# Kernel optimization log

Hardware: AMD Instinct MI355X
Metric: run time of the kernel (lower is better)

The kernel has to match this reference:

```python
import jax, jax.numpy as jnp
import numpy as np

D_MODEL = 1024
D_STATE = 16
N_LAYERS = 2
EXPAND = 2
D_CONV = 4
D_INNER = EXPAND * D_MODEL
DT_RANK = D_MODEL // 16  # 64
B, L = 2, 1024


def setup_inputs() -> dict:
    key = jax.random.key(0)
    ks = jax.random.split(key, 8)
    rn = lambda k, shape, s: jax.random.normal(k, shape, jnp.float32) * s
    x = rn(ks[0], (B, L, D_MODEL), 1.0)
    in_proj_w = rn(ks[1], (N_LAYERS, 2 * D_INNER, D_MODEL), D_MODEL ** -0.5)
    conv_w = rn(ks[2], (N_LAYERS, D_INNER, 1, D_CONV), D_CONV ** -0.5)
    conv_b = jnp.zeros((N_LAYERS, D_INNER), jnp.float32)
    x_proj_w = rn(ks[3], (N_LAYERS, DT_RANK + 2 * D_STATE, D_INNER), D_INNER ** -0.5)
    dt_proj_w = rn(ks[4], (N_LAYERS, D_INNER, DT_RANK), DT_RANK ** -0.5)
    dt_proj_b = rn(ks[5], (N_LAYERS, D_INNER), 0.1)
    # canonical Mamba init: A = -exp(A_log), A_log = log(1..d_state)
    A_log = jnp.tile(jnp.log(jnp.arange(1, D_STATE + 1, dtype=jnp.float32)), (N_LAYERS, D_INNER, 1))
    Dp = jnp.ones((N_LAYERS, D_INNER), jnp.float32)
    out_proj_w = rn(ks[6], (N_LAYERS, D_MODEL, D_INNER), D_INNER ** -0.5)
    ln_g = jnp.ones((N_LAYERS, D_MODEL), jnp.float32)
    ln_b = jnp.zeros((N_LAYERS, D_MODEL), jnp.float32)
    fn_g = jnp.ones((D_MODEL,), jnp.float32)
    fn_b = jnp.zeros((D_MODEL,), jnp.float32)
    return dict(x=x, ln_g=ln_g, ln_b=ln_b, in_proj_w=in_proj_w, conv_w=conv_w,
                conv_b=conv_b, x_proj_w=x_proj_w, dt_proj_w=dt_proj_w,
                dt_proj_b=dt_proj_b, A_log=A_log, Dp=Dp, out_proj_w=out_proj_w,
                fn_g=fn_g, fn_b=fn_b)


def _ln(x, g, b):
    m = jnp.mean(x, -1, keepdims=True)
    v = jnp.mean((x - m) ** 2, -1, keepdims=True)
    return (x - m) * jax.lax.rsqrt(v + 1e-5) * g + b


def _mamba_block(x, in_w, cw, cb, xpw, dtw, dtb, A_log, Dp, ow):
    Bb = x.shape[0]
    # input projection -> [B, L, 2*d_inner]
    xz = jnp.einsum('bld,ed->ble', x, in_w)
    u, res = jnp.split(xz, 2, axis=-1)
    # causal depthwise conv over time (torch: padding=3 then [..., :L])
    uc = jax.lax.conv_general_dilated(
        u.transpose(0, 2, 1), cw, (1,), [(D_CONV - 1, 0)],
        dimension_numbers=('NCH', 'OIH', 'NCH'), feature_group_count=D_INNER)
    u = jax.nn.silu(uc.transpose(0, 2, 1) + cb)  # [B, L, d_inner]
    # input-dependent dt, B, C
    xdbl = jnp.einsum('ble,fe->blf', u, xpw)
    dt, Bc, Cc = jnp.split(xdbl, [DT_RANK, DT_RANK + D_STATE], axis=-1)
    delta = jax.nn.softplus(jnp.einsum('blr,dr->bld', dt, dtw) + dtb)  # [B,L,d_inner]
    A = -jnp.exp(A_log)  # [d_inner, d_state]

    def step(h, inp):
        d_t, B_t, C_t, u_t = inp  # [B,d_inner],[B,d_state],[B,d_state],[B,d_inner]
        h = jnp.exp(d_t[:, :, None] * A) * h + (d_t * u_t)[:, :, None] * B_t[:, None, :]
        y = jnp.einsum('bds,bs->bd', h, C_t)
        return h, y

    xs = (delta.transpose(1, 0, 2), Bc.transpose(1, 0, 2),
          Cc.transpose(1, 0, 2), u.transpose(1, 0, 2))
    h0 = jnp.zeros((Bb, D_INNER, D_STATE), x.dtype)
    _, ys = jax.lax.scan(step, h0, xs)
    y = ys.transpose(1, 0, 2) + u * Dp
    y = y * jax.nn.silu(res)
    return jnp.einsum('ble,de->bld', y, ow)


def reference(x, ln_g, ln_b, in_proj_w, conv_w, conv_b, x_proj_w, dt_proj_w,
              dt_proj_b, A_log, Dp, out_proj_w, fn_g, fn_b):
    for i in range(N_LAYERS):
        x = x + _mamba_block(_ln(x, ln_g[i], ln_b[i]), in_proj_w[i], conv_w[i],
                             conv_b[i], x_proj_w[i], dt_proj_w[i], dt_proj_b[i],
                             A_log[i], Dp[i], out_proj_w[i])
    # dropout is identity in eval mode
    return _ln(x, fn_g, fn_b)
```

## Files before the change

kernel.cpp:

```cpp
#include <hip/hip_runtime.h>
#include <hip/hip_bf16.h>
#include <math.h>
#include <stdint.h>

#define DMODEL 1024
#define DSTATE 16
#define DINNER 2048
#define DTRANK 64
#define NB 2
#define LSEQ 1024
#define ROWS (NB*LSEQ)
#define NCH 64
#define LCH (LSEQ/NCH)

typedef __bf16 bf16_t;
typedef __bf16 bf16x8 __attribute__((ext_vector_type(8)));
typedef __bf16 bf16x4 __attribute__((ext_vector_type(4)));
typedef float  f32x4  __attribute__((ext_vector_type(4)));

#define AS1(p) ((const __attribute__((address_space(1))) void*)(p))
#define AS3(p) ((__attribute__((address_space(3))) void*)(uint32_t)(uintptr_t)(p))

static __device__ __forceinline__ float sigmoidf_(float x){ return 1.f/(1.f+__expf(-x)); }
static __device__ __forceinline__ float softplusf_(float x){ return fmaxf(x,0.f) + log1pf(__expf(-fabsf(x))); }

__global__ __launch_bounds__(256) void cvt_kernel(const float* __restrict__ in,
    bf16_t* __restrict__ out, int n4)
{
  int i = blockIdx.x*256 + threadIdx.x;
  if (i < n4){
    float4 v = ((const float4*)in)[i];
    bf16x4 o = { (bf16_t)v.x, (bf16_t)v.y, (bf16_t)v.z, (bf16_t)v.w };
    ((bf16x4*)out)[i] = o;
  }
}

template<int OUTBF>
__global__ __launch_bounds__(256) void ln_kernel(const float* __restrict__ x,
    const float* __restrict__ g, const float* __restrict__ b,
    float* __restrict__ outf, bf16_t* __restrict__ outb)
{
  int row = blockIdx.x;
  float4 v = ((const float4*)(x + (size_t)row*DMODEL))[threadIdx.x];
  float s  = v.x+v.y+v.z+v.w;
  float s2 = v.x*v.x+v.y*v.y+v.z*v.z+v.w*v.w;
  #pragma unroll
  for (int off=32; off>=1; off>>=1){ s += __shfl_xor(s,off); s2 += __shfl_xor(s2,off); }
  __shared__ float red[8];
  int lane = threadIdx.x & 63, wid = threadIdx.x >> 6;
  if (lane==0){ red[wid]=s; red[4+wid]=s2; }
  __syncthreads();
  float ts  = red[0]+red[1]+red[2]+red[3];
  float ts2 = red[4]+red[5]+red[6]+red[7];
  float mean = ts*(1.f/DMODEL);
  float var  = ts2*(1.f/DMODEL) - mean*mean;
  float rstd = rsqrtf(var + 1e-5f);
  float4 gv = ((const float4*)g)[threadIdx.x];
  float4 bv = ((const float4*)b)[threadIdx.x];
  float4 o;
  o.x=(v.x-mean)*rstd*gv.x+bv.x;
  o.y=(v.y-mean)*rstd*gv.y+bv.y;
  o.z=(v.z-mean)*rstd*gv.z+bv.z;
  o.w=(v.w-mean)*rstd*gv.w+bv.w;
  if (OUTBF){
    bf16x4 ob = { (bf16_t)o.x, (bf16_t)o.y, (bf16_t)o.z, (bf16_t)o.w };
    ((bf16x4*)(outb + (size_t)row*DMODEL))[threadIdx.x] = ob;
  } else {
    ((float4*)(outf + (size_t)row*DMODEL))[threadIdx.x] = o;
  }
}

#define GBM 128
#define GBN 128
#define GBK 64

template<int EPI, bool NGUARD>
__global__ __launch_bounds__(256) void gemm_bf16(
    const bf16_t* __restrict__ A, int lda,
    const bf16_t* __restrict__ W, int ldw,
    float* __restrict__ C, int ldc,
    int M, int N, int K,
    const float* __restrict__ bias,
    const float* __restrict__ addsrc,
    bf16_t* __restrict__ C2)
{
  __shared__ __align__(16) char lds[2*GBM*GBK*2];
  char* sA = lds;
  char* sB = lds + GBM*GBK*2;
  const int tid  = threadIdx.x;
  const int lane = tid & 63, wid = tid >> 6;
  const int wr = wid >> 1, wc = wid & 1;
  const int frow = lane & 15, kgrp = lane >> 4;
  const int m0 = blockIdx.y*GBM, n0 = blockIdx.x*GBN;
  const int srow  = (lane >> 3);
  const int scolb = (lane & 7) * 16;

  f32x4 acc[4][4];
  #pragma unroll
  for (int i=0;i<4;i++)
    #pragma unroll
    for (int j=0;j<4;j++)
      acc[i][j] = (f32x4){0.f,0.f,0.f,0.f};

  for (int k0 = 0; k0 < K; k0 += GBK) {
    #pragma unroll
    for (int r=0;r<4;++r){
      int ci  = r*4 + wid;
      int row = ci*8 + srow;
      {
        const char* src = (const char*)A + ((size_t)(m0+row)*lda + k0)*2 + scolb;
        __builtin_amdgcn_global_load_lds(AS1(src), AS3(sA + ci*1024), 16, 0, 0);
      }
      {
        int grow = n0 + row;
        if (NGUARD) grow = (grow < N) ? grow : (N-1);
        const char* src = (const char*)W + ((size_t)grow*ldw + k0)*2 + scolb;
        __builtin_amdgcn_global_load_lds(AS1(src), AS3(sB + ci*1024), 16, 0, 0);
      }
    }
    __syncthreads();
    #pragma unroll
    for (int ks=0; ks<2; ++ks){
      bf16x8 af[4], bfr[4];
      #pragma unroll
      for (int i=0;i<4;i++)
        af[i] = *(const bf16x8*)(sA + (wr*64 + i*16 + frow)*128 + ks*64 + kgrp*16);
      #pragma unroll
      for (int j=0;j<4;j++)
        bfr[j] = *(const bf16x8*)(sB + (wc*64 + j*16 + frow)*128 + ks*64 + kgrp*16);
      #pragma unroll
      for (int i=0;i<4;i++)
        #pragma unroll
        for (int j=0;j<4;j++)
          acc[i][j] = __builtin_amdgcn_mfma_f32_16x16x32_bf16(af[i], bfr[j], acc[i][j], 0, 0, 0);
    }
    __syncthreads();
  }

  #pragma unroll
  for (int i=0;i<4;i++){
    int rbase = m0 + wr*64 + i*16 + kgrp*4;
    #pragma unroll
    for (int j=0;j<4;j++){
      int col = n0 + wc*64 + j*16 + frow;
      if (NGUARD && col >= N) continue;
      #pragma unroll
      for (int q=0;q<4;q++){
        float v = acc[i][j][q];
        int row = rbase + q;
        if (EPI==1) v = softplusf_(v + bias[col]);
        if (EPI==2) v += addsrc[(size_t)row*ldc + col];
        C[(size_t)row*ldc + col] = v;
        if (EPI==3) C2[(size_t)row*ldc + col] = (bf16_t)v;
      }
    }
  }
}

__global__ __launch_bounds__(256) void conv_silu_kernel(
    const float* __restrict__ xz, const float* __restrict__ cw,
    const float* __restrict__ cb, float* __restrict__ u, bf16_t* __restrict__ ub)
{
  int idx = blockIdx.x*256 + threadIdx.x;
  int d  = idx & (DINNER-1);
  int bl = idx >> 11;
  int l  = bl & (LSEQ-1);
  const float* col = xz + (size_t)bl*(2*DINNER) + d;
  float w0=cw[d*4+0], w1=cw[d*4+1], w2=cw[d*4+2], w3=cw[d*4+3];
  float x3 = col[0];
  float x2 = (l>=1) ? col[-(ptrdiff_t)(2*DINNER)]  : 0.f;
  float x1 = (l>=2) ? col[-(ptrdiff_t)(4*DINNER)]  : 0.f;
  float x0 = (l>=3) ? col[-(ptrdiff_t)(6*DINNER)]  : 0.f;
  float acc = cb[d] + w0*x0 + w1*x1 + w2*x2 + w3*x3;
  float uu = acc * sigmoidf_(acc);
  u [(size_t)bl*DINNER + d] = uu;
  ub[(size_t)bl*DINNER + d] = (bf16_t)uu;
}

__global__ __launch_bounds__(256) void scan_phase1(
    const float* __restrict__ delta, const float* __restrict__ u,
    const float* __restrict__ xdbl, const float* __restrict__ A_log,
    float* __restrict__ hout, float* __restrict__ sumd)
{
  int gid = blockIdx.x*256 + threadIdx.x;
  int d = gid & (DINNER-1);
  int c = (gid >> 11) & (NCH-1);
  int b = gid >> 17;
  float A[DSTATE];
  #pragma unroll
  for (int s=0;s<DSTATE;s++) A[s] = -__expf(A_log[d*DSTATE+s]);
  int l0 = c*LCH;
  const float* drow = delta + ((size_t)(b*LSEQ + l0))*DINNER + d;
  const float* urow = u     + ((size_t)(b*LSEQ + l0))*DINNER + d;
  const float* xrow = xdbl  + ((size_t)(b*LSEQ + l0))*96 + DTRANK;
  float h[DSTATE] = {};
  float sd = 0.f;
  for (int l=0; l<LCH; ++l) {
    float dv = drow[(size_t)l*DINNER];
    float uv = urow[(size_t)l*DINNER];
    const float* bc = xrow + l*96;
    float du = dv*uv;
    sd += dv;
    #pragma unroll
    for (int s=0;s<DSTATE;s++)
      h[s] = __expf(dv*A[s])*h[s] + du*bc[s];
  }
  float* hp = hout + (((size_t)(b*NCH + c))*DINNER + d)*DSTATE;
  #pragma unroll
  for (int q=0;q<4;q++)
    ((float4*)hp)[q] = make_float4(h[4*q],h[4*q+1],h[4*q+2],h[4*q+3]);
  sumd[((size_t)(b*NCH + c))*DINNER + d] = sd;
}

__global__ __launch_bounds__(256) void scan_phase2(
    float* __restrict__ hout, const float* __restrict__ sumd,
    const float* __restrict__ A_log)
{
  int gid = blockIdx.x*256 + threadIdx.x;
  int s = gid & (DSTATE-1);
  int d = (gid >> 4) & (DINNER-1);
  int b = gid >> 15;
  float A = -__expf(A_log[d*DSTATE+s]);
  float h = 0.f;
  for (int c=0; c<NCH; ++c) {
    size_t hi = (((size_t)(b*NCH + c))*DINNER + d)*DSTATE + s;
    float tmp = hout[hi];
    hout[hi] = h;
    float P = __expf(A * sumd[((size_t)(b*NCH + c))*DINNER + d]);
    h = P*h + tmp;
  }
}

__global__ __launch_bounds__(256) void scan_phase3(
    const float* __restrict__ delta, bf16_t* __restrict__ ysb,
    const float* __restrict__ u,
    const float* __restrict__ xz,
    const float* __restrict__ xdbl,
    const float* __restrict__ A_log,
    const float* __restrict__ Dp,
    const float* __restrict__ hin)
{
  int gid = blockIdx.x*256 + threadIdx.x;
  int d = gid & (DINNER-1);
  int c = (gid >> 11) & (NCH-1);
  int b = gid >> 17;
  float A[DSTATE];
  #pragma unroll
  for (int s=0;s<DSTATE;s++) A[s] = -__expf(A_log[d*DSTATE+s]);
  float Dpd = Dp[d];
  float h[DSTATE];
  const float* hp = hin + (((size_t)(b*NCH + c))*DINNER + d)*DSTATE;
  #pragma unroll
  for (int q=0;q<4;q++){
    float4 hv = ((const float4*)hp)[q];
    h[4*q]=hv.x; h[4*q+1]=hv.y; h[4*q+2]=hv.z; h[4*q+3]=hv.w;
  }
  int l0 = c*LCH;
  const float* drow = delta + ((size_t)(b*LSEQ + l0))*DINNER + d;
  const float* urow = u     + ((size_t)(b*LSEQ + l0))*DINNER + d;
  const float* rrow = xz    + ((size_t)(b*LSEQ + l0))*2*DINNER + DINNER + d;
  const float* xrow = xdbl  + ((size_t)(b*LSEQ + l0))*96 + DTRANK;
  bf16_t* yrow = ysb + ((size_t)(b*LSEQ + l0))*DINNER + d;
  for (int l=0; l<LCH; ++l) {
    float dv = drow[(size_t)l*DINNER];
    float uv = urow[(size_t)l*DINNER];
    float rv = rrow[(size_t)l*2*DINNER];
    const float* bc = xrow + l*96;
    float du = dv*uv;
    float y = 0.f;
    #pragma unroll
    for (int s=0;s<DSTATE;s++){
      float dA = __expf(dv*A[s]);
      h[s] = dA*h[s] + du*bc[s];
      y += h[s]*bc[DSTATE+s];
    }
    y = (y + uv*Dpd) * (rv * sigmoidf_(rv));
    yrow[(size_t)l*DINNER] = (bf16_t)y;
  }
}

extern "C" void kernel_launch(void* const* d_in, const int* in_sizes, int n_in,
                              void* d_out, int out_size, void* d_ws, size_t ws_size,
                              hipStream_t stream)
{
  const float* x      = (const float*)d_in[0];
  const float* ln_g   = (const float*)d_in[1];
  const float* ln_b   = (const float*)d_in[2];
  const float* in_w   = (const float*)d_in[3];
  const float* conv_w = (const float*)d_in[4];
  const float* conv_b = (const float*)d_in[5];
  const float* xp_w   = (const float*)d_in[6];
  const float* dt_w   = (const float*)d_in[7];
  const float* dt_b   = (const float*)d_in[8];
  const float* A_log  = (const float*)d_in[9];
  const float* Dp     = (const float*)d_in[10];
  const float* out_w  = (const float*)d_in[11];
  const float* fn_g   = (const float*)d_in[12];
  const float* fn_b   = (const float*)d_in[13];
  float* out = (float*)d_out;

  char* p = (char*)d_ws;
  auto alloc = [&](size_t bytes)->char*{ char* r = p; p += (bytes + 255) & ~(size_t)255; return r; };

  const size_t N_INW = (size_t)2*2*DINNER*DMODEL;
  const size_t N_XPW = (size_t)2*96*DINNER;
  const size_t N_DTW = (size_t)2*DINNER*DTRANK;
  const size_t N_OUTW= (size_t)2*DMODEL*DINNER;

  bf16_t* inw_b  = (bf16_t*)alloc(N_INW*2);
  bf16_t* xpw_b  = (bf16_t*)alloc(N_XPW*2);
  bf16_t* dtw_b  = (bf16_t*)alloc(N_DTW*2);
  bf16_t* outw_b = (bf16_t*)alloc(N_OUTW*2);
  float*  x_cur  = (float*) alloc((size_t)ROWS*DMODEL*4);
  bf16_t* xn_b   = (bf16_t*)alloc((size_t)ROWS*DMODEL*2);
  float*  xz     = (float*) alloc((size_t)ROWS*2*DINNER*4);
  float*  ubuf   = (float*) alloc((size_t)ROWS*DINNER*4);
  bf16_t* ub_b   = (bf16_t*)alloc((size_t)ROWS*DINNER*2);
  float*  xdbl   = (float*) alloc((size_t)ROWS*96*4);
  bf16_t* xdbl_b = (bf16_t*)alloc((size_t)ROWS*96*2);
  float*  delta  = (float*) alloc((size_t)ROWS*DINNER*4);
  float*  hout   = (float*) alloc((size_t)NB*NCH*DINNER*DSTATE*4);
  float*  sumd   = (float*) alloc((size_t)NB*NCH*DINNER*4);
  bf16_t* ys_b   = ub_b;

  cvt_kernel<<<(int)((N_INW/4 +255)/256),256,0,stream>>>(in_w,  inw_b,  (int)(N_INW/4));
  cvt_kernel<<<(int)((N_XPW/4 +255)/256),256,0,stream>>>(xp_w,  xpw_b,  (int)(N_XPW/4));
  cvt_kernel<<<(int)((N_DTW/4 +255)/256),256,0,stream>>>(dt_w,  dtw_b,  (int)(N_DTW/4));
  cvt_kernel<<<(int)((N_OUTW/4+255)/256),256,0,stream>>>(out_w, outw_b, (int)(N_OUTW/4));

  for (int layer=0; layer<2; ++layer) {
    const float* xin = (layer==0) ? x : x_cur;
    const float* Al  = A_log + (size_t)layer*DINNER*DSTATE;
    ln_kernel<1><<<ROWS,256,0,stream>>>(xin, ln_g+layer*DMODEL, ln_b+layer*DMODEL, nullptr, xn_b);
    gemm_bf16<0,false><<<dim3(2*DINNER/GBN, ROWS/GBM),256,0,stream>>>(
        xn_b, DMODEL, inw_b + (size_t)layer*2*DINNER*DMODEL, DMODEL,
        xz, 2*DINNER, ROWS, 2*DINNER, DMODEL, nullptr, nullptr, nullptr);
    conv_silu_kernel<<<(ROWS*DINNER)/256,256,0,stream>>>(
        xz, conv_w + (size_t)layer*DINNER*4, conv_b + (size_t)layer*DINNER, ubuf, ub_b);
    gemm_bf16<3,true><<<dim3(1, ROWS/GBM),256,0,stream>>>(
        ub_b, DINNER, xpw_b + (size_t)layer*96*DINNER, DINNER,
        xdbl, 96, ROWS, 96, DINNER, nullptr, nullptr, xdbl_b);
    gemm_bf16<1,false><<<dim3(DINNER/GBN, ROWS/GBM),256,0,stream>>>(
        xdbl_b, 96, dtw_b + (size_t)layer*DINNER*DTRANK, DTRANK,
        delta, DINNER, ROWS, DINNER, DTRANK,
        dt_b + (size_t)layer*DINNER, nullptr, nullptr);
    scan_phase1<<<(NB*NCH*DINNER)/256,256,0,stream>>>(delta, ubuf, xdbl, Al, hout, sumd);
    scan_phase2<<<(NB*DINNER*DSTATE)/256,256,0,stream>>>(hout, sumd, Al);
    scan_phase3<<<(NB*NCH*DINNER)/256,256,0,stream>>>(
        delta, ys_b, ubuf, xz, xdbl, Al, Dp + (size_t)layer*DINNER, hout);
    gemm_bf16<2,false><<<dim3(DMODEL/GBN, ROWS/GBM),256,0,stream>>>(
        ys_b, DINNER, outw_b + (size_t)layer*DMODEL*DINNER, DINNER,
        x_cur, DMODEL, ROWS, DMODEL, DINNER, nullptr, xin, nullptr);
  }
  ln_kernel<0><<<ROWS,256,0,stream>>>(x_cur, fn_g, fn_b, out, nullptr);
}
```

Measured before the change: 541.2 us.

## Store xz and u in bf16, split-K x_proj, swizzle GEMM blocks, halve scan chunks

```diff
diff --git a/kernel.cpp b/kernel.cpp
--- a/kernel.cpp
+++ b/kernel.cpp
@@ -10,8 +10,9 @@
 #define NB 2
 #define LSEQ 1024
 #define ROWS (NB*LSEQ)
-#define NCH 64
+#define NCH 32
 #define LCH (LSEQ/NCH)
+#define KSPLIT 8
 
 typedef __bf16 bf16_t;
 typedef __bf16 bf16x8 __attribute__((ext_vector_type(8)));
@@ -74,7 +75,7 @@
 #define GBN 128
 #define GBK 64
 
-template<int EPI, bool NGUARD>
+template<int EPI, bool NGUARD, bool SWZ>
 __global__ __launch_bounds__(256) void gemm_bf16(
     const bf16_t* __restrict__ A, int lda,
     const bf16_t* __restrict__ W, int ldw,
@@ -91,7 +92,20 @@
   const int lane = tid & 63, wid = tid >> 6;
   const int wr = wid >> 1, wc = wid & 1;
   const int frow = lane & 15, kgrp = lane >> 4;
-  const int m0 = blockIdx.y*GBM, n0 = blockIdx.x*GBN;
+
+  int bx = blockIdx.x, by = blockIdx.y;
+  if (SWZ) {
+    int gx = gridDim.x, gy = gridDim.y;
+    int bid = by*gx + bx;
+    int q = (gx*gy) >> 3;
+    int nid = (bid & 7)*q + (bid >> 3);
+    int stripH = gy << 3;
+    int strip = nid / stripH;
+    int rem   = nid % stripH;
+    bx = (strip << 3) + (rem & 7);
+    by = rem >> 3;
+  }
+  const int m0 = by*GBM, n0 = bx*GBN;
   const int srow  = (lane >> 3);
   const int scolb = (lane & 7) * 16;
 
@@ -102,7 +116,9 @@
     for (int j=0;j<4;j++)
       acc[i][j] = (f32x4){0.f,0.f,0.f,0.f};
 
-  for (int k0 = 0; k0 < K; k0 += GBK) {
+  const int ksl = K / gridDim.z;
+  const int kb  = blockIdx.z * ksl;
+  for (int k0 = kb; k0 < kb + ksl; k0 += GBK) {
     #pragma unroll
     for (int r=0;r<4;++r){
       int ci  = r*4 + wid;
@@ -137,6 +153,37 @@
     __syncthreads();
   }
 
+  if (EPI==4) {
+    #pragma unroll
+    for (int i=0;i<4;i++){
+      int rbase = wr*64 + i*16 + kgrp*4;
+      #pragma unroll
+      for (int j=0;j<4;j++){
+        int col = wc*64 + j*16 + frow;
+        #pragma unroll
+        for (int q=0;q<4;q++){
+          int row = rbase + q;
+          int byte = (row<<8) + (col<<1);
+          byte ^= (row & 7) << 4;
+          *(bf16_t*)(lds + byte) = (bf16_t)acc[i][j][q];
+        }
+      }
+    }
+    __syncthreads();
+    int r = tid >> 1;
+    int hb = (tid & 1) << 7;
+    size_t gbase = (size_t)(m0 + r)*ldc + n0 + ((tid & 1) << 6);
+    #pragma unroll
+    for (int i=0;i<8;i++){
+      int byte = (r<<8) + hb + (i<<4);
+      byte ^= (r & 7) << 4;
+      bf16x8 v = *(const bf16x8*)(lds + byte);
+      *(bf16x8*)(C2 + gbase + (i<<3)) = v;
+    }
+    return;
+  }
+
+  float* Cw = (EPI==5) ? (C + (size_t)blockIdx.z*(size_t)M*ldc) : C;
   #pragma unroll
   for (int i=0;i<4;i++){
     int rbase = m0 + wr*64 + i*16 + kgrp*4;
@@ -150,54 +197,63 @@
         int row = rbase + q;
         if (EPI==1) v = softplusf_(v + bias[col]);
         if (EPI==2) v += addsrc[(size_t)row*ldc + col];
-        C[(size_t)row*ldc + col] = v;
-        if (EPI==3) C2[(size_t)row*ldc + col] = (bf16_t)v;
+        Cw[(size_t)row*ldc + col] = v;
       }
     }
   }
 }
 
+__global__ __launch_bounds__(256) void xp_reduce(
+    const float* __restrict__ part, float* __restrict__ xdbl, bf16_t* __restrict__ xdbl_b)
+{
+  int idx = blockIdx.x*256 + threadIdx.x;
+  float s = 0.f;
+  #pragma unroll
+  for (int k=0;k<KSPLIT;k++) s += part[(size_t)k*ROWS*96 + idx];
+  xdbl[idx] = s;
+  xdbl_b[idx] = (bf16_t)s;
+}
+
 __global__ __launch_bounds__(256) void conv_silu_kernel(
-    const float* __restrict__ xz, const float* __restrict__ cw,
-    const float* __restrict__ cb, float* __restrict__ u, bf16_t* __restrict__ ub)
+    const bf16_t* __restrict__ xzb, const float* __restrict__ cw,
+    const float* __restrict__ cb, bf16_t* __restrict__ ub)
 {
   int idx = blockIdx.x*256 + threadIdx.x;
   int d  = idx & (DINNER-1);
   int bl = idx >> 11;
   int l  = bl & (LSEQ-1);
-  const float* col = xz + (size_t)bl*(2*DINNER) + d;
+  const bf16_t* col = xzb + (size_t)bl*(2*DINNER) + d;
   float w0=cw[d*4+0], w1=cw[d*4+1], w2=cw[d*4+2], w3=cw[d*4+3];
-  float x3 = col[0];
-  float x2 = (l>=1) ? col[-(ptrdiff_t)(2*DINNER)]  : 0.f;
-  float x1 = (l>=2) ? col[-(ptrdiff_t)(4*DINNER)]  : 0.f;
-  float x0 = (l>=3) ? col[-(ptrdiff_t)(6*DINNER)]  : 0.f;
+  float x3 = (float)col[0];
+  float x2 = (l>=1) ? (float)col[-(ptrdiff_t)(2*DINNER)]  : 0.f;
+  float x1 = (l>=2) ? (float)col[-(ptrdiff_t)(4*DINNER)]  : 0.f;
+  float x0 = (l>=3) ? (float)col[-(ptrdiff_t)(6*DINNER)]  : 0.f;
   float acc = cb[d] + w0*x0 + w1*x1 + w2*x2 + w3*x3;
   float uu = acc * sigmoidf_(acc);
-  u [(size_t)bl*DINNER + d] = uu;
   ub[(size_t)bl*DINNER + d] = (bf16_t)uu;
 }
 
 __global__ __launch_bounds__(256) void scan_phase1(
-    const float* __restrict__ delta, const float* __restrict__ u,
+    const float* __restrict__ delta, const bf16_t* __restrict__ u,
     const float* __restrict__ xdbl, const float* __restrict__ A_log,
     float* __restrict__ hout, float* __restrict__ sumd)
 {
   int gid = blockIdx.x*256 + threadIdx.x;
   int d = gid & (DINNER-1);
   int c = (gid >> 11) & (NCH-1);
-  int b = gid >> 17;
+  int b = gid >> 16;
   float A[DSTATE];
   #pragma unroll
   for (int s=0;s<DSTATE;s++) A[s] = -__expf(A_log[d*DSTATE+s]);
   int l0 = c*LCH;
-  const float* drow = delta + ((size_t)(b*LSEQ + l0))*DINNER + d;
-  const float* urow = u     + ((size_t)(b*LSEQ + l0))*DINNER + d;
-  const float* xrow = xdbl  + ((size_t)(b*LSEQ + l0))*96 + DTRANK;
+  const float*  drow = delta + ((size_t)(b*LSEQ + l0))*DINNER + d;
+  const bf16_t* urow = u     + ((size_t)(b*LSEQ + l0))*DINNER + d;
+  const float*  xrow = xdbl  + ((size_t)(b*LSEQ + l0))*96 + DTRANK;
   float h[DSTATE] = {};
   float sd = 0.f;
   for (int l=0; l<LCH; ++l) {
     float dv = drow[(size_t)l*DINNER];
-    float uv = urow[(size_t)l*DINNER];
+    float uv = (float)urow[(size_t)l*DINNER];
     const float* bc = xrow + l*96;
     float du = dv*uv;
     sd += dv;
@@ -232,9 +288,9 @@
 }
 
 __global__ __launch_bounds__(256) void scan_phase3(
-    const float* __restrict__ delta, bf16_t* __restrict__ ysb,
-    const float* __restrict__ u,
-    const float* __restrict__ xz,
+    const float* __restrict__ delta, bf16_t* ysb,
+    const bf16_t* u,
+    const bf16_t* __restrict__ xzb,
     const float* __restrict__ xdbl,
     const float* __restrict__ A_log,
     const float* __restrict__ Dp,
@@ -243,7 +299,7 @@
   int gid = blockIdx.x*256 + threadIdx.x;
   int d = gid & (DINNER-1);
   int c = (gid >> 11) & (NCH-1);
-  int b = gid >> 17;
+  int b = gid >> 16;
   float A[DSTATE];
   #pragma unroll
   for (int s=0;s<DSTATE;s++) A[s] = -__expf(A_log[d*DSTATE+s]);
@@ -256,15 +312,15 @@
     h[4*q]=hv.x; h[4*q+1]=hv.y; h[4*q+2]=hv.z; h[4*q+3]=hv.w;
   }
   int l0 = c*LCH;
-  const float* drow = delta + ((size_t)(b*LSEQ + l0))*DINNER + d;
-  const float* urow = u     + ((size_t)(b*LSEQ + l0))*DINNER + d;
-  const float* rrow = xz    + ((size_t)(b*LSEQ + l0))*2*DINNER + DINNER + d;
-  const float* xrow = xdbl  + ((size_t)(b*LSEQ + l0))*96 + DTRANK;
+  const float*  drow = delta + ((size_t)(b*LSEQ + l0))*DINNER + d;
+  const bf16_t* urow = u     + ((size_t)(b*LSEQ + l0))*DINNER + d;
+  const bf16_t* rrow = xzb   + ((size_t)(b*LSEQ + l0))*2*DINNER + DINNER + d;
+  const float*  xrow = xdbl  + ((size_t)(b*LSEQ + l0))*96 + DTRANK;
   bf16_t* yrow = ysb + ((size_t)(b*LSEQ + l0))*DINNER + d;
   for (int l=0; l<LCH; ++l) {
     float dv = drow[(size_t)l*DINNER];
-    float uv = urow[(size_t)l*DINNER];
-    float rv = rrow[(size_t)l*2*DINNER];
+    float uv = (float)urow[(size_t)l*DINNER];
+    float rv = (float)rrow[(size_t)l*2*DINNER];
     const float* bc = xrow + l*96;
     float du = dv*uv;
     float y = 0.f;
@@ -313,11 +369,11 @@
   bf16_t* outw_b = (bf16_t*)alloc(N_OUTW*2);
   float*  x_cur  = (float*) alloc((size_t)ROWS*DMODEL*4);
   bf16_t* xn_b   = (bf16_t*)alloc((size_t)ROWS*DMODEL*2);
-  float*  xz     = (float*) alloc((size_t)ROWS*2*DINNER*4);
-  float*  ubuf   = (float*) alloc((size_t)ROWS*DINNER*4);
+  bf16_t* xzb    = (bf16_t*)alloc((size_t)ROWS*2*DINNER*2);
   bf16_t* ub_b   = (bf16_t*)alloc((size_t)ROWS*DINNER*2);
   float*  xdbl   = (float*) alloc((size_t)ROWS*96*4);
   bf16_t* xdbl_b = (bf16_t*)alloc((size_t)ROWS*96*2);
+  float*  xpart  = (float*) alloc((size_t)KSPLIT*ROWS*96*4);
   float*  delta  = (float*) alloc((size_t)ROWS*DINNER*4);
   float*  hout   = (float*) alloc((size_t)NB*NCH*DINNER*DSTATE*4);
   float*  sumd   = (float*) alloc((size_t)NB*NCH*DINNER*4);
@@ -332,23 +388,24 @@
     const float* xin = (layer==0) ? x : x_cur;
     const float* Al  = A_log + (size_t)layer*DINNER*DSTATE;
     ln_kernel<1><<<ROWS,256,0,stream>>>(xin, ln_g+layer*DMODEL, ln_b+layer*DMODEL, nullptr, xn_b);
-    gemm_bf16<0,false><<<dim3(2*DINNER/GBN, ROWS/GBM),256,0,stream>>>(
+    gemm_bf16<4,false,true><<<dim3(2*DINNER/GBN, ROWS/GBM),256,0,stream>>>(
         xn_b, DMODEL, inw_b + (size_t)layer*2*DINNER*DMODEL, DMODEL,
-        xz, 2*DINNER, ROWS, 2*DINNER, DMODEL, nullptr, nullptr, nullptr);
+        nullptr, 2*DINNER, ROWS, 2*DINNER, DMODEL, nullptr, nullptr, xzb);
     conv_silu_kernel<<<(ROWS*DINNER)/256,256,0,stream>>>(
-        xz, conv_w + (size_t)layer*DINNER*4, conv_b + (size_t)layer*DINNER, ubuf, ub_b);
-    gemm_bf16<3,true><<<dim3(1, ROWS/GBM),256,0,stream>>>(
+        xzb, conv_w + (size_t)layer*DINNER*4, conv_b + (size_t)layer*DINNER, ub_b);
+    gemm_bf16<5,true,false><<<dim3(1, ROWS/GBM, KSPLIT),256,0,stream>>>(
         ub_b, DINNER, xpw_b + (size_t)layer*96*DINNER, DINNER,
-        xdbl, 96, ROWS, 96, DINNER, nullptr, nullptr, xdbl_b);
-    gemm_bf16<1,false><<<dim3(DINNER/GBN, ROWS/GBM),256,0,stream>>>(
+        xpart, 96, ROWS, 96, DINNER, nullptr, nullptr, nullptr);
+    xp_reduce<<<(ROWS*96)/256,256,0,stream>>>(xpart, xdbl, xdbl_b);
+    gemm_bf16<1,false,true><<<dim3(DINNER/GBN, ROWS/GBM),256,0,stream>>>(
         xdbl_b, 96, dtw_b + (size_t)layer*DINNER*DTRANK, DTRANK,
         delta, DINNER, ROWS, DINNER, DTRANK,
         dt_b + (size_t)layer*DINNER, nullptr, nullptr);
-    scan_phase1<<<(NB*NCH*DINNER)/256,256,0,stream>>>(delta, ubuf, xdbl, Al, hout, sumd);
+    scan_phase1<<<(NB*NCH*DINNER)/256,256,0,stream>>>(delta, ub_b, xdbl, Al, hout, sumd);
     scan_phase2<<<(NB*DINNER*DSTATE)/256,256,0,stream>>>(hout, sumd, Al);
     scan_phase3<<<(NB*NCH*DINNER)/256,256,0,stream>>>(
-        delta, ys_b, ubuf, xz, xdbl, Al, Dp + (size_t)layer*DINNER, hout);
-    gemm_bf16<2,false><<<dim3(DMODEL/GBN, ROWS/GBM),256,0,stream>>>(
+        delta, ys_b, ub_b, xzb, xdbl, Al, Dp + (size_t)layer*DINNER, hout);
+    gemm_bf16<2,false,true><<<dim3(DMODEL/GBN, ROWS/GBM),256,0,stream>>>(
         ys_b, DINNER, outw_b + (size_t)layer*DMODEL*DINNER, DINNER,
         x_cur, DMODEL, ROWS, DMODEL, DINNER, nullptr, xin, nullptr);
   }
```

After: 547.4 us. No clear change (+1.1%).
